# Kernel tuning notes

Measured on AMD Instinct MI355X. Metric: run time of the kernel, lower is better.

## Reference

```python
import jax, jax.numpy as jnp
import numpy as np

B, L, D, DK, T = 8192, 64, 512, 64, 128
WIDE_IN = 2 * T + T * T  # 16640


def setup_inputs() -> dict:
    key = jax.random.key(0)
    ks = jax.random.split(key, 24)
    s = 0.02
    inp = {
        "mashup_tags": jax.random.uniform(ks[0], (B, T), jnp.float32),
        "target_api_tags": jax.random.uniform(ks[1], (B, T), jnp.float32),
        "cross_product_tag": jax.random.uniform(ks[2], (B, T * T), jnp.float32),
        "encoded_api_context": jax.random.normal(ks[3], (B, L, D), jnp.float32),
        "candidate_api_description_feature": jax.random.normal(ks[4], (B, D), jnp.float32),
        "mashup_description_feature": jax.random.normal(ks[5], (B, D), jnp.float32),
        "context_len": jax.random.randint(ks[6], (B,), 0, L + 1, jnp.int64 if jax.config.jax_enable_x64 else jnp.int32),
        # attention projections (torch Linear weight layout: [out, in], no bias)
        "W_K": s * jax.random.normal(ks[7], (DK, D), jnp.float32),
        "W_Q": s * jax.random.normal(ks[8], (DK, D), jnp.float32),
        # wide head
        "wide_w": s * jax.random.normal(ks[9], (1, WIDE_IN), jnp.float32),
        "wide_b": jnp.zeros((1,), jnp.float32),
        # deep MLP 1536->512->256->128->1
        "d1_w": s * jax.random.normal(ks[10], (512, 3 * D), jnp.float32),
        "d1_b": jnp.zeros((512,), jnp.float32),
        "d2_w": s * jax.random.normal(ks[11], (256, 512), jnp.float32),
        "d2_b": jnp.zeros((256,), jnp.float32),
        "d3_w": s * jax.random.normal(ks[12], (128, 256), jnp.float32),
        "d3_b": jnp.zeros((128,), jnp.float32),
        "d4_w": s * jax.random.normal(ks[13], (1, 128), jnp.float32),
        "d4_b": jnp.zeros((1,), jnp.float32),
        "wide_weight": jnp.ones((1,), jnp.float32),
        "deep_weight": jnp.ones((1,), jnp.float32),
        "bias": jnp.zeros((1,), jnp.float32),
    }
    return inp


def reference(mashup_tags, target_api_tags, cross_product_tag,
              encoded_api_context, candidate_api_description_feature,
              mashup_description_feature, context_len,
              W_K, W_Q, wide_w, wide_b,
              d1_w, d1_b, d2_w, d2_b, d3_w, d3_b, d4_w, d4_b,
              wide_weight, deep_weight, bias):
    # ---- wide branch ----
    wide_in = jnp.concatenate([mashup_tags, target_api_tags, cross_product_tag], axis=1)
    wide_out = jax.nn.sigmoid(wide_in @ wide_w.T + wide_b)  # (B,1)

    # ---- ragged attention (vectorized masked softmax replaces the Python batch loop) ----
    K = jnp.einsum("bld,kd->blk", encoded_api_context, W_K)          # (B,L,dk)
    Q = candidate_api_description_feature @ W_Q.T                     # (B,dk)
    scores = jnp.einsum("blk,bk->bl", K, Q)                           # (B,L)
    mask = jnp.arange(scores.shape[1])[None, :] < context_len[:, None]
    m = jnp.max(jnp.where(mask, scores, -1e30), axis=-1, keepdims=True)
    e = jnp.where(mask, jnp.exp(scores - m), 0.0)
    denom = jnp.sum(e, axis=-1, keepdims=True)
    probs = e / jnp.maximum(denom, 1e-30)  # rows with length==0 -> all zeros (matches torch zeros fallback)
    api_context = jnp.einsum("bl,bld->bd", probs, encoded_api_context)  # (B,512)

    # ---- deep branch ----
    deep_in = jnp.concatenate([mashup_description_feature, api_context,
                               candidate_api_description_feature], axis=1)  # (B,1536)
    h = jax.nn.relu(deep_in @ d1_w.T + d1_b)
    h = jax.nn.relu(h @ d2_w.T + d2_b)
    h = jax.nn.relu(h @ d3_w.T + d3_b)
    deep_out = h @ d4_w.T + d4_b  # (B,1)

    out = wide_weight * wide_out + deep_weight * deep_out + bias
    return jax.nn.sigmoid(out)
```

## Files before the change

### kernel.cpp

```cpp
#include <hip/hip_runtime.h>

#define Bsz 8192
#define Lctx 64
#define Ddim 512
#define DK 64
#define Ttag 128
#define RQT 4

using f32x4 = __attribute__((ext_vector_type(4))) float;
using bf16x8 = __attribute__((ext_vector_type(8))) short;

__device__ __forceinline__ float wave_sum(float v) {
#pragma unroll
    for (int m = 32; m > 0; m >>= 1) v += __shfl_xor(v, m, 64);
    return v;
}

__device__ __forceinline__ float dot4(float4 a, float4 b) {
    return a.x * b.x + a.y * b.y + a.z * b.z + a.w * b.w;
}

__device__ __forceinline__ unsigned f2bf(float f) {
    unsigned int u = __float_as_uint(f);
    u = u + 0x7fffu + ((u >> 16) & 1u);
    return u >> 16;
}
__device__ __forceinline__ unsigned pack2(float a, float b) {
    return f2bf(a) | (f2bf(b) << 16);
}

__global__ __launch_bounds__(256) void k_prep(
    const float* __restrict__ C, const float* __restrict__ WQ,
    const float* __restrict__ WK, float* __restrict__ qt,
    const float* __restrict__ s1, unsigned short* __restrict__ d1,
    const float* __restrict__ s2, unsigned short* __restrict__ d2,
    const float* __restrict__ s3, unsigned short* __restrict__ d3)
{
    if (blockIdx.x >= 512) {
        int i = (blockIdx.x - 512) * 256 + threadIdx.x;
        const float* s;
        unsigned short* d;
        if (i < 196608)      { s = s1; d = d1; }
        else if (i < 229376) { i -= 196608; s = s2; d = d2; }
        else                 { i -= 229376; s = s3; d = d3; }
        const float4 v = ((const float4*)s)[i];
        uint2 w;
        w.x = pack2(v.x, v.y);
        w.y = pack2(v.z, v.w);
        *(uint2*)&d[(size_t)i * 4] = w;
        return;
    }

    const int lane = threadIdx.x & 63;
    const int gw = blockIdx.x * 4 + (threadIdx.x >> 6);
    const int b0 = gw * RQT;

    float4 c0[RQT], c1[RQT];
#pragma unroll
    for (int r = 0; r < RQT; ++r) {
        const float4* row = (const float4*)(C + (size_t)(b0 + r) * Ddim);
        c0[r] = row[lane];
        c1[r] = row[64 + lane];
    }
    float tv[RQT];
#pragma unroll
    for (int r = 0; r < RQT; ++r) tv[r] = 0.f;
    for (int k = 0; k < DK; ++k) {
        const float4* wrow = (const float4*)(WQ + (size_t)k * Ddim);
        const float4 w0 = wrow[lane];
        const float4 w1 = wrow[64 + lane];
#pragma unroll
        for (int r = 0; r < RQT; ++r) {
            float p = dot4(c0[r], w0) + dot4(c1[r], w1);
            p = wave_sum(p);
            if (lane == k) tv[r] = p;
        }
    }
    float4 a0[RQT], a1[RQT];
#pragma unroll
    for (int r = 0; r < RQT; ++r) {
        a0[r] = make_float4(0.f, 0.f, 0.f, 0.f);
        a1[r] = make_float4(0.f, 0.f, 0.f, 0.f);
    }
    for (int k = 0; k < DK; ++k) {
        const float4* wrow = (const float4*)(WK + (size_t)k * Ddim);
        const float4 w0 = wrow[lane];
        const float4 w1 = wrow[64 + lane];
#pragma unroll
        for (int r = 0; r < RQT; ++r) {
            const float tk = __shfl(tv[r], k, 64);
            a0[r].x += tk * w0.x; a0[r].y += tk * w0.y;
            a0[r].z += tk * w0.z; a0[r].w += tk * w0.w;
            a1[r].x += tk * w1.x; a1[r].y += tk * w1.y;
            a1[r].z += tk * w1.z; a1[r].w += tk * w1.w;
        }
    }
#pragma unroll
    for (int r = 0; r < RQT; ++r) {
        float4* orow = (float4*)(qt + (size_t)(b0 + r) * Ddim);
        orow[lane] = a0[r];
        orow[64 + lane] = a1[r];
    }
}

__global__ __launch_bounds__(256) void k_big(
    const float* __restrict__ X, const float* __restrict__ qt,
    const int* __restrict__ clen, const float* __restrict__ mdesc,
    const float* __restrict__ cand,
    const float* __restrict__ mt, const float* __restrict__ tt,
    const float* __restrict__ cp, const float* __restrict__ ww,
    const float* __restrict__ wb,
    unsigned short* __restrict__ din, float* __restrict__ wl)
{
    const int g = blockIdx.x;
    const int kind = (g >> 3) & 1;
    const int idx = (int)(((g >> 4) << 3) | (g & 7));
    const int tid = threadIdx.x;
    const int wave = tid >> 6, lane = tid & 63;
    const int b = idx * 4 + wave;

    if (kind == 1) {
        float wacc;
        {
            const float2 a  = ((const float2*)(mt + (size_t)b * Ttag))[lane];
            const float2 wA = ((const float2*)ww)[lane];
            const float2 t  = ((const float2*)(tt + (size_t)b * Ttag))[lane];
            const float2 wB = ((const float2*)(ww + Ttag))[lane];
            wacc = a.x * wA.x + a.y * wA.y + t.x * wB.x + t.y * wB.y;
        }
        const float4* cp4 = (const float4*)(cp + (size_t)b * (Ttag * Ttag));
        const float4* ww4 = (const float4*)(ww + 2 * Ttag);
        float w0 = 0.f, w1 = 0.f;
#pragma unroll 8
        for (int i = 0; i < 64; i += 2) {
            w0 += dot4(cp4[i * 64 + lane],       ww4[i * 64 + lane]);
            w1 += dot4(cp4[(i + 1) * 64 + lane], ww4[(i + 1) * 64 + lane]);
        }
        wacc += w0 + w1;
        wacc = wave_sum(wacc);
        if (lane == 0) wl[b] = wacc + wb[0];
        return;
    }

    const int len = clen[b];
    const float4* qrow = (const float4*)(qt + (size_t)b * Ddim);
    const float4 q0 = qrow[lane];
    const float4 q1 = qrow[64 + lane];
    const float4* xb = (const float4*)(X + (size_t)b * Lctx * Ddim);

    float4 y0 = make_float4(0.f, 0.f, 0.f, 0.f);
    float4 y1 = make_float4(0.f, 0.f, 0.f, 0.f);
    float M = -1e30f, D = 0.f;

    const int nch = (len + 7) >> 3;
    for (int c = 0; c < nch; ++c) {
        const int base = c * 8;
        const int nr = min(8, len - base);
        float4 t0[8], t1[8];
#pragma unroll
        for (int r = 0; r < 8; ++r) {
            const int l = base + min(r, nr - 1);
            t0[r] = xb[l * 128 + lane];
            t1[r] = xb[l * 128 + 64 + lane];
        }
        float sc[8];
#pragma unroll
        for (int r = 0; r < 8; ++r)
            if (r < nr) sc[r] = dot4(t0[r], q0) + dot4(t1[r], q1);
#pragma unroll
        for (int r = 0; r < 8; ++r)
            if (r < nr) sc[r] = wave_sum(sc[r]);

        float pmax = -1e30f;
#pragma unroll
        for (int r = 0; r < 8; ++r)
            if (r < nr) pmax = fmaxf(pmax, sc[r]);
        const float Mn = fmaxf(M, pmax);
        const float scale = __expf(M - Mn);
        D *= scale;
        y0.x *= scale; y0.y *= scale; y0.z *= scale; y0.w *= scale;
        y1.x *= scale; y1.y *= scale; y1.z *= scale; y1.w *= scale;
#pragma unroll
        for (int r = 0; r < 8; ++r) {
            if (r < nr) {
                const float e = __expf(sc[r] - Mn);
                D += e;
                y0.x += e * t0[r].x; y0.y += e * t0[r].y;
                y0.z += e * t0[r].z; y0.w += e * t0[r].w;
                y1.x += e * t1[r].x; y1.y += e * t1[r].y;
                y1.z += e * t1[r].z; y1.w += e * t1[r].w;
            }
        }
        M = Mn;
    }

    unsigned short* dr = din + (size_t)b * 1536;
    const float rden = 1.f / fmaxf(D, 1e-30f);
    {
        uint2 w;
        w.x = pack2(y0.x * rden, y0.y * rden);
        w.y = pack2(y0.z * rden, y0.w * rden);
        *(uint2*)&dr[512 + 4 * lane] = w;
        w.x = pack2(y1.x * rden, y1.y * rden);
        w.y = pack2(y1.z * rden, y1.w * rden);
        *(uint2*)&dr[512 + 256 + 4 * lane] = w;
    }
    {
        const float4* md = (const float4*)(mdesc + (size_t)b * Ddim);
        const float4 m0 = md[lane], m1 = md[64 + lane];
        uint2 w;
        w.x = pack2(m0.x, m0.y); w.y = pack2(m0.z, m0.w);
        *(uint2*)&dr[4 * lane] = w;
        w.x = pack2(m1.x, m1.y); w.y = pack2(m1.z, m1.w);
        *(uint2*)&dr[256 + 4 * lane] = w;
    }
    {
        const float4* cd = (const float4*)(cand + (size_t)b * Ddim);
        const float4 c0 = cd[lane], c1 = cd[64 + lane];
        uint2 w;
        w.x = pack2(c0.x, c0.y); w.y = pack2(c0.z, c0.w);
        *(uint2*)&dr[1024 + 4 * lane] = w;
        w.x = pack2(c1.x, c1.y); w.y = pack2(c1.z, c1.w);
        *(uint2*)&dr[1024 + 256 + 4 * lane] = w;
    }
}

template <int BN>
__global__ __launch_bounds__(256) void k_gemm_bf16(
    const unsigned short* __restrict__ A, const unsigned short* __restrict__ W,
    const float* __restrict__ bias, unsigned short* __restrict__ C,
    const int K, const int N, const int relu)
{
    constexpr int WN = BN / 2;
    constexpr int NN = WN / 16;
    constexpr int NB = (BN * 8) / 256;
    __shared__ unsigned short As[128][72];
    __shared__ unsigned short Bs[BN][72];
    const int tid = threadIdx.x;
    const int wave = tid >> 6, lane = tid & 63;
    const int wm = wave >> 1, wn = wave & 1;
    const size_t m0 = (size_t)blockIdx.x * 128;
    const size_t n0 = (size_t)blockIdx.y * BN;

    f32x4 acc[4][NN];
#pragma unroll
    for (int i = 0; i < 4; ++i)
#pragma unroll
        for (int j = 0; j < NN; ++j) acc[i][j] = (f32x4){0.f, 0.f, 0.f, 0.f};

    uint4 pa[4], pb[NB];
    auto loadA = [&](int k0) {
#pragma unroll
        for (int j = 0; j < 4; ++j) {
            const int i = tid + j * 256;
            const int row = i >> 3, c8 = (i & 7) * 8;
            pa[j] = *(const uint4*)(A + (m0 + row) * (size_t)K + k0 + c8);
        }
    };
    auto loadB = [&](int k0) {
#pragma unroll
        for (int j = 0; j < NB; ++j) {
            const int i = tid + j * 256;
            const int row = i >> 3, c8 = (i & 7) * 8;
            pb[j] = *(const uint4*)(W + (n0 + row) * (size_t)K + k0 + c8);
        }
    };

    loadA(0);
    loadB(0);
    for (int k0 = 0; k0 < K; k0 += 64) {
        __syncthreads();
#pragma unroll
        for (int j = 0; j < 4; ++j) {
            const int i = tid + j * 256;
            const int row = i >> 3, c8 = (i & 7) * 8;
            *(uint4*)&As[row][c8] = pa[j];
        }
#pragma unroll
        for (int j = 0; j < NB; ++j) {
            const int i = tid + j * 256;
            const int row = i >> 3, c8 = (i & 7) * 8;
            *(uint4*)&Bs[row][c8] = pb[j];
        }
        __syncthreads();
        if (k0 + 64 < K) { loadA(k0 + 64); loadB(k0 + 64); }
#pragma unroll
        for (int kk = 0; kk < 2; ++kk) {
            const int krow = kk * 32 + (lane >> 4) * 8;
            bf16x8 af[4], bfr[NN];
#pragma unroll
            for (int mm = 0; mm < 4; ++mm)
                af[mm] = *(const bf16x8*)&As[wm * 64 + mm * 16 + (lane & 15)][krow];
#pragma unroll
            for (int nn = 0; nn < NN; ++nn)
                bfr[nn] = *(const bf16x8*)&Bs[wn * WN + nn * 16 + (lane & 15)][krow];
#pragma unroll
            for (int mm = 0; mm < 4; ++mm)
#pragma unroll
                for (int nn = 0; nn < NN; ++nn)
                    acc[mm][nn] = __builtin_amdgcn_mfma_f32_16x16x32_bf16(
                        af[mm], bfr[nn], acc[mm][nn], 0, 0, 0);
        }
    }

#pragma unroll
    for (int nn = 0; nn < NN; ++nn) {
        const int col = (int)n0 + wn * WN + nn * 16 + (lane & 15);
        const float bv = bias[col];
#pragma unroll
        for (int mm = 0; mm < 4; ++mm) {
#pragma unroll
            for (int r = 0; r < 4; ++r) {
                const size_t row = m0 + wm * 64 + mm * 16 + (lane >> 4) * 4 + r;
                float v = acc[mm][nn][r] + bv;
                if (relu) v = fmaxf(v, 0.f);
                C[row * N + col] = (unsigned short)f2bf(v);
            }
        }
    }
}

__global__ __launch_bounds__(256) void k_gemm3_final(
    const unsigned short* __restrict__ A, const unsigned short* __restrict__ W,
    const float* __restrict__ bias, const float* __restrict__ d4w,
    const float* __restrict__ d4b, const float* __restrict__ wl,
    const float* __restrict__ wwt, const float* __restrict__ dwt,
    const float* __restrict__ bs, float* __restrict__ out)
{
    constexpr int K = 256, N = 128;
    __shared__ unsigned short As[128][72];
    __shared__ unsigned short Bs[128][72];
    __shared__ float dp[128][2];
    const int tid = threadIdx.x;
    const int wave = tid >> 6, lane = tid & 63;
    const int wm = wave >> 1, wn = wave & 1;
    const size_t m0 = (size_t)blockIdx.x * 128;

    f32x4 acc[4][4];
#pragma unroll
    for (int i = 0; i < 4; ++i)
#pragma unroll
        for (int j = 0; j < 4; ++j) acc[i][j] = (f32x4){0.f, 0.f, 0.f, 0.f};

    uint4 pa[4], pb[4];
    auto loadA = [&](int k0) {
#pragma unroll
        for (int j = 0; j < 4; ++j) {
            const int i = tid + j * 256;
            const int row = i >> 3, c8 = (i & 7) * 8;
            pa[j] = *(const uint4*)(A + (m0 + row) * (size_t)K + k0 + c8);
        }
    };
    auto loadB = [&](int k0) {
#pragma unroll
        for (int j = 0; j < 4; ++j) {
            const int i = tid + j * 256;
            const int row = i >> 3, c8 = (i & 7) * 8;
            pb[j] = *(const uint4*)(W + row * (size_t)K + k0 + c8);
        }
    };

    loadA(0);
    loadB(0);
    for (int k0 = 0; k0 < K; k0 += 64) {
        __syncthreads();
#pragma unroll
        for (int j = 0; j < 4; ++j) {
            const int i = tid + j * 256;
            const int row = i >> 3, c8 = (i & 7) * 8;
            *(uint4*)&As[row][c8] = pa[j];
            *(uint4*)&Bs[row][c8] = pb[j];
        }
        __syncthreads();
        if (k0 + 64 < K) { loadA(k0 + 64); loadB(k0 + 64); }
#pragma unroll
        for (int kk = 0; kk < 2; ++kk) {
            const int krow = kk * 32 + (lane >> 4) * 8;
            bf16x8 af[4], bfr[4];
#pragma unroll
            for (int mm = 0; mm < 4; ++mm)
                af[mm] = *(const bf16x8*)&As[wm * 64 + mm * 16 + (lane & 15)][krow];
#pragma unroll
            for (int nn = 0; nn < 4; ++nn)
                bfr[nn] = *(const bf16x8*)&Bs[wn * 64 + nn * 16 + (lane & 15)][krow];
#pragma unroll
            for (int mm = 0; mm < 4; ++mm)
#pragma unroll
                for (int nn = 0; nn < 4; ++nn)
                    acc[mm][nn] = __builtin_amdgcn_mfma_f32_16x16x32_bf16(
                        af[mm], bfr[nn], acc[mm][nn], 0, 0, 0);
        }
    }

    float rowpart[4][4];
#pragma unroll
    for (int mm = 0; mm < 4; ++mm)
#pragma unroll
        for (int r = 0; r < 4; ++r) rowpart[mm][r] = 0.f;
#pragma unroll
    for (int nn = 0; nn < 4; ++nn) {
        const int col = wn * 64 + nn * 16 + (lane & 15);
        const float bv = bias[col];
        const float w4 = d4w[col];
#pragma unroll
        for (int mm = 0; mm < 4; ++mm)
#pragma unroll
            for (int r = 0; r < 4; ++r) {
                float v = acc[mm][nn][r] + bv;
                v = fmaxf(v, 0.f);
                rowpart[mm][r] += v * w4;
            }
    }
#pragma unroll
    for (int mm = 0; mm < 4; ++mm)
#pragma unroll
        for (int r = 0; r < 4; ++r) {
            float v = rowpart[mm][r];
            v += __shfl_xor(v, 1, 64);
            v += __shfl_xor(v, 2, 64);
            v += __shfl_xor(v, 4, 64);
            v += __shfl_xor(v, 8, 64);
            if ((lane & 15) == 0)
                dp[wm * 64 + mm * 16 + (lane >> 4) * 4 + r][wn] = v;
        }
    __syncthreads();
    if (tid < 128) {
        const int row = tid;
        const float deep = dp[row][0] + dp[row][1] + d4b[0];
        const size_t b = m0 + row;
        const float wo = 1.f / (1.f + __expf(-wl[b]));
        const float z = wwt[0] * wo + dwt[0] * deep + bs[0];
        out[b] = 1.f / (1.f + __expf(-z));
    }
}

extern "C" void kernel_launch(void* const* d_in, const int* in_sizes, int n_in,
                              void* d_out, int out_size, void* d_ws, size_t ws_size,
                              hipStream_t stream)
{
    const float* mt    = (const float*)d_in[0];
    const float* tt    = (const float*)d_in[1];
    const float* cp    = (const float*)d_in[2];
    const float* X     = (const float*)d_in[3];
    const float* cand  = (const float*)d_in[4];
    const float* mdesc = (const float*)d_in[5];
    const int*   clen  = (const int*)d_in[6];
    const float* WK    = (const float*)d_in[7];
    const float* WQ    = (const float*)d_in[8];
    const float* ww    = (const float*)d_in[9];
    const float* wb    = (const float*)d_in[10];
    const float* d1w   = (const float*)d_in[11];
    const float* d1b   = (const float*)d_in[12];
    const float* d2w   = (const float*)d_in[13];
    const float* d2b   = (const float*)d_in[14];
    const float* d3w   = (const float*)d_in[15];
    const float* d3b   = (const float*)d_in[16];
    const float* d4w   = (const float*)d_in[17];
    const float* d4b   = (const float*)d_in[18];
    const float* wwt   = (const float*)d_in[19];
    const float* dwt   = (const float*)d_in[20];
    const float* bs    = (const float*)d_in[21];
    float* out = (float*)d_out;

    char* w = (char*)d_ws;
    unsigned short* din = (unsigned short*)w;            w += (size_t)Bsz * 1536 * 2;
    float* qt           = (float*)w;                     w += (size_t)Bsz * 512 * 4;
    unsigned short* h1  = (unsigned short*)w;            w += (size_t)Bsz * 512 * 2;
    unsigned short* h2  = (unsigned short*)w;            w += (size_t)Bsz * 256 * 2;
    float* wl           = (float*)w;                     w += (size_t)Bsz * 4;
    unsigned short* w1b = (unsigned short*)w;            w += (size_t)512 * 1536 * 2;
    unsigned short* w2b = (unsigned short*)w;            w += (size_t)256 * 512 * 2;
    unsigned short* w3b = (unsigned short*)w;            w += (size_t)128 * 256 * 2;

    hipLaunchKernelGGL(k_prep, dim3(1440), dim3(256), 0, stream,
                       cand, WQ, WK, qt, d1w, w1b, d2w, w2b, d3w, w3b);
    hipLaunchKernelGGL(k_big, dim3(4096), dim3(256), 0, stream,
                       X, qt, clen, mdesc, cand, mt, tt, cp, ww, wb, din, wl);
    hipLaunchKernelGGL((k_gemm_bf16<64>), dim3(64, 8), dim3(256), 0, stream,
                       din, w1b, d1b, h1, 1536, 512, 1);
    hipLaunchKernelGGL((k_gemm_bf16<64>), dim3(64, 4), dim3(256), 0, stream,
                       h1, w2b, d2b, h2, 512, 256, 1);
    hipLaunchKernelGGL(k_gemm3_final, dim3(64), dim3(256), 0, stream,
                       h2, w3b, d3b, d4w, d4b, wl, wwt, dwt, bs, out);
}
```

Baseline: 445.9 us.

## Fuse wide-branch dot product into attention loop within each wave

Replaces the interleaved block-kind split, where separate blocks handled the attention and wide branches, with one kernel in which each wave streams both its attention context rows and its cross-product row in the same loop. The chunk size drops from 8 rows to 4 so the cross-product loads fit alongside the context loads. The goal is to balance memory traffic per wave and hide latency on the variable-length attention part. The grid is halved, and each wave now always does the full 64 KB cross-product stream, so the load per wave is more even but per-wave time goes up. Smaller chunks also mean more wave reductions per row.

```diff
diff --git a/kernel.cpp b/kernel.cpp
--- a/kernel.cpp
+++ b/kernel.cpp
@@ -103,7 +103,7 @@
     }
 }
 
-__global__ __launch_bounds__(256) void k_big(
+__global__ __launch_bounds__(256) void k_attn_wide(
     const float* __restrict__ X, const float* __restrict__ qt,
     const int* __restrict__ clen, const float* __restrict__ mdesc,
     const float* __restrict__ cand,
@@ -112,87 +112,87 @@
     const float* __restrict__ wb,
     unsigned short* __restrict__ din, float* __restrict__ wl)
 {
-    const int g = blockIdx.x;
-    const int kind = (g >> 3) & 1;
-    const int idx = (int)(((g >> 4) << 3) | (g & 7));
     const int tid = threadIdx.x;
     const int wave = tid >> 6, lane = tid & 63;
-    const int b = idx * 4 + wave;
-
-    if (kind == 1) {
-        float wacc;
-        {
-            const float2 a  = ((const float2*)(mt + (size_t)b * Ttag))[lane];
-            const float2 wA = ((const float2*)ww)[lane];
-            const float2 t  = ((const float2*)(tt + (size_t)b * Ttag))[lane];
-            const float2 wB = ((const float2*)(ww + Ttag))[lane];
-            wacc = a.x * wA.x + a.y * wA.y + t.x * wB.x + t.y * wB.y;
-        }
-        const float4* cp4 = (const float4*)(cp + (size_t)b * (Ttag * Ttag));
-        const float4* ww4 = (const float4*)(ww + 2 * Ttag);
-        float w0 = 0.f, w1 = 0.f;
-#pragma unroll 8
-        for (int i = 0; i < 64; i += 2) {
-            w0 += dot4(cp4[i * 64 + lane],       ww4[i * 64 + lane]);
-            w1 += dot4(cp4[(i + 1) * 64 + lane], ww4[(i + 1) * 64 + lane]);
-        }
-        wacc += w0 + w1;
-        wacc = wave_sum(wacc);
-        if (lane == 0) wl[b] = wacc + wb[0];
-        return;
-    }
-
+    const int b = blockIdx.x * 4 + wave;
     const int len = clen[b];
+
     const float4* qrow = (const float4*)(qt + (size_t)b * Ddim);
     const float4 q0 = qrow[lane];
     const float4 q1 = qrow[64 + lane];
     const float4* xb = (const float4*)(X + (size_t)b * Lctx * Ddim);
+    const float4* cp4 = (const float4*)(cp + (size_t)b * (Ttag * Ttag));
+    const float4* ww4 = (const float4*)(ww + 2 * Ttag);
+
+    float wacc;
+    {
+        const float2 a  = ((const float2*)(mt + (size_t)b * Ttag))[lane];
+        const float2 wA = ((const float2*)ww)[lane];
+        const float2 t  = ((const float2*)(tt + (size_t)b * Ttag))[lane];
+        const float2 wB = ((const float2*)(ww + Ttag))[lane];
+        wacc = a.x * wA.x + a.y * wA.y + t.x * wB.x + t.y * wB.y;
+    }
 
     float4 y0 = make_float4(0.f, 0.f, 0.f, 0.f);
     float4 y1 = make_float4(0.f, 0.f, 0.f, 0.f);
     float M = -1e30f, D = 0.f;
 
-    const int nch = (len + 7) >> 3;
-    for (int c = 0; c < nch; ++c) {
-        const int base = c * 8;
-        const int nr = min(8, len - base);
-        float4 t0[8], t1[8];
-#pragma unroll
-        for (int r = 0; r < 8; ++r) {
-            const int l = base + min(r, nr - 1);
-            t0[r] = xb[l * 128 + lane];
-            t1[r] = xb[l * 128 + 64 + lane];
-        }
-        float sc[8];
-#pragma unroll
-        for (int r = 0; r < 8; ++r)
-            if (r < nr) sc[r] = dot4(t0[r], q0) + dot4(t1[r], q1);
-#pragma unroll
-        for (int r = 0; r < 8; ++r)
-            if (r < nr) sc[r] = wave_sum(sc[r]);
-
-        float pmax = -1e30f;
-#pragma unroll
-        for (int r = 0; r < 8; ++r)
-            if (r < nr) pmax = fmaxf(pmax, sc[r]);
-        const float Mn = fmaxf(M, pmax);
-        const float scale = __expf(M - Mn);
-        D *= scale;
-        y0.x *= scale; y0.y *= scale; y0.z *= scale; y0.w *= scale;
-        y1.x *= scale; y1.y *= scale; y1.z *= scale; y1.w *= scale;
-#pragma unroll
-        for (int r = 0; r < 8; ++r) {
-            if (r < nr) {
-                const float e = __expf(sc[r] - Mn);
-                D += e;
-                y0.x += e * t0[r].x; y0.y += e * t0[r].y;
-                y0.z += e * t0[r].z; y0.w += e * t0[r].w;
-                y1.x += e * t1[r].x; y1.y += e * t1[r].y;
-                y1.z += e * t1[r].z; y1.w += e * t1[r].w;
+    for (int c = 0; c < 16; ++c) {
+        const int base = c * 4;
+        const int nr = min(4, len - base);
+
+        float4 t0[4], t1[4];
+        if (nr > 0) {
+#pragma unroll
+            for (int r = 0; r < 4; ++r) {
+                const int l = base + min(r, nr - 1);
+                t0[r] = xb[l * 128 + lane];
+                t1[r] = xb[l * 128 + 64 + lane];
             }
         }
-        M = Mn;
-    }
+        float4 cv[4], wv[4];
+#pragma unroll
+        for (int i = 0; i < 4; ++i) {
+            cv[i] = cp4[(c * 4 + i) * 64 + lane];
+            wv[i] = ww4[(c * 4 + i) * 64 + lane];
+        }
+
+        if (nr > 0) {
+            float sc[4];
+#pragma unroll
+            for (int r = 0; r < 4; ++r)
+                sc[r] = dot4(t0[r], q0) + dot4(t1[r], q1);
+#pragma unroll
+            for (int r = 0; r < 4; ++r) sc[r] = wave_sum(sc[r]);
+
+            float pmax = -1e30f;
+#pragma unroll
+            for (int r = 0; r < 4; ++r)
+                if (r < nr) pmax = fmaxf(pmax, sc[r]);
+            const float Mn = fmaxf(M, pmax);
+            const float scale = __expf(M - Mn);
+            D *= scale;
+            y0.x *= scale; y0.y *= scale; y0.z *= scale; y0.w *= scale;
+            y1.x *= scale; y1.y *= scale; y1.z *= scale; y1.w *= scale;
+#pragma unroll
+            for (int r = 0; r < 4; ++r) {
+                if (r < nr) {
+                    const float e = __expf(sc[r] - Mn);
+                    D += e;
+                    y0.x += e * t0[r].x; y0.y += e * t0[r].y;
+                    y0.z += e * t0[r].z; y0.w += e * t0[r].w;
+                    y1.x += e * t1[r].x; y1.y += e * t1[r].y;
+                    y1.z += e * t1[r].z; y1.w += e * t1[r].w;
+                }
+            }
+            M = Mn;
+        }
+#pragma unroll
+        for (int i = 0; i < 4; ++i) wacc += dot4(cv[i], wv[i]);
+    }
+
+    wacc = wave_sum(wacc);
+    if (lane == 0) wl[b] = wacc + wb[0];
 
     unsigned short* dr = din + (size_t)b * 1536;
     const float rden = 1.f / fmaxf(D, 1e-30f);
@@ -474,7 +474,7 @@
 
     hipLaunchKernelGGL(k_prep, dim3(1440), dim3(256), 0, stream,
                        cand, WQ, WK, qt, d1w, w1b, d2w, w2b, d3w, w3b);
-    hipLaunchKernelGGL(k_big, dim3(4096), dim3(256), 0, stream,
+    hipLaunchKernelGGL(k_attn_wide, dim3(Bsz / 4), dim3(256), 0, stream,
                        X, qt, clen, mdesc, cand, mt, tt, cp, ww, wb, din, wl);
     hipLaunchKernelGGL((k_gemm_bf16<64>), dim3(64, 8), dim3(256), 0, stream,
                        din, w1b, d1b, h1, 1536, 512, 1);
```

After: 451.6 us. No clear change (+1.3%).
